# Optimization experiments

Hardware: AMD Instinct MI355X
Metric: run time of the kernel (lower is better)

Reference implementation:

```python
import jax, jax.numpy as jnp
import numpy as np

N = 50000      # nodes
E = 800000     # edges
GENE = 64      # gene_dim
HID = 128      # hidden_dim
NCLS = 10      # num_classes
EPS = 1e-5


def setup_inputs() -> dict:
    key = jax.random.key(0)
    ks = jax.random.split(key, 4)
    inp = {
        "x": jax.random.normal(ks[0], (N, GENE), jnp.float32),
        "edge_index": jax.random.randint(ks[1], (2, E), 0, N),
    }
    # PNA-style conv: concat([x, 4 aggregators x 3 scalers]) -> 13*d_in features
    dims = [(GENE, HID), (HID, 2 * HID), (2 * HID, HID), (HID, HID // 2)]
    for i, (din, dout) in enumerate(dims, 1):
        k = jax.random.fold_in(key, i)
        inp[f"W{i}"] = jax.random.normal(k, (13 * din, dout), jnp.float32) / float(np.sqrt(13 * din))
        inp[f"b{i}"] = jnp.zeros((dout,), jnp.float32)
        inp[f"gamma{i}"] = jnp.ones((dout,), jnp.float32)
        inp[f"beta{i}"] = jnp.zeros((dout,), jnp.float32)
    inp["Wc"] = jax.random.normal(ks[2], (HID // 2, NCLS), jnp.float32) / float(np.sqrt(HID // 2))
    inp["bc"] = jnp.zeros((NCLS,), jnp.float32)
    return inp


def _pna(x, src, dst, deg, log_deg, delta, W, b):
    # gather source features along edges: [E, d]
    msg = x[src]
    cnt = jnp.maximum(deg, 1.0)[:, None]
    s = jax.ops.segment_sum(msg, dst, num_segments=N)
    mean = s / cnt
    mean_sq = jax.ops.segment_sum(msg * msg, dst, num_segments=N) / cnt
    std = jnp.sqrt(jnp.maximum(mean_sq - mean * mean, 0.0) + EPS)
    has = (deg > 0)[:, None]
    mn = jnp.where(has, jax.ops.segment_min(msg, dst, num_segments=N), 0.0)
    mx = jnp.where(has, jax.ops.segment_max(msg, dst, num_segments=N), 0.0)
    aggs = jnp.concatenate([mean, mn, mx, std], axis=-1)  # [N, 4d]
    amp = (log_deg / delta)[:, None]                       # amplification scaler
    att = jnp.where(log_deg > 0, delta / jnp.maximum(log_deg, 1e-6), 1.0)[:, None]
    feat = jnp.concatenate([x, aggs, aggs * amp, aggs * att], axis=-1)  # [N, 13d]
    return feat @ W + b


def _bn(h, gamma, beta):
    m = h.mean(axis=0)
    v = h.var(axis=0)
    return (h - m) / jnp.sqrt(v + EPS) * gamma + beta


def reference(x, edge_index, W1, b1, gamma1, beta1, W2, b2, gamma2, beta2,
              W3, b3, gamma3, beta3, W4, b4, gamma4, beta4, Wc, bc):
    src, dst = edge_index[0], edge_index[1]
    deg = jax.ops.segment_sum(jnp.ones((E,), jnp.float32), dst, num_segments=N)
    log_deg = jnp.log1p(deg)
    delta = log_deg.mean()
    h = _pna(x, src, dst, deg, log_deg, delta, W1, b1)
    h = _bn(jax.nn.relu(h), gamma1, beta1)
    h = _pna(h, src, dst, deg, log_deg, delta, W2, b2)
    h = _bn(jax.nn.relu(h), gamma2, beta2)
    h = _pna(h, src, dst, deg, log_deg, delta, W3, b3)
    h = _bn(jax.nn.relu(h), gamma3, beta3)
    h = _pna(h, src, dst, deg, log_deg, delta, W4, b4)
    h = _bn(jax.nn.relu(h), gamma4, beta4)
    return h @ Wc + bc
```

## Files before the change

kernel.cpp:

```cpp
#include <hip/hip_runtime.h>
#include <hip/hip_bf16.h>

#define NN 50000
#define NE 800000
#define EPSV 1e-5f
#define NB 49

typedef _Float16 h8 __attribute__((ext_vector_type(8)));
typedef float    f4 __attribute__((ext_vector_type(4)));

#define AS1 __attribute__((address_space(1)))
#define AS3 __attribute__((address_space(3)))

__device__ __forceinline__ void gload_lds16(const _Float16* g, _Float16* l){
  __builtin_amdgcn_global_load_lds((const AS1 void*)g, (AS3 void*)l, 16, 0, 0);
}


__global__ void k_deg(const int* __restrict__ dst, int* __restrict__ deg){
  int e = blockIdx.x*blockDim.x + threadIdx.x;
  if(e < NE) atomicAdd(&deg[dst[e]], 1);
}

__global__ void k_logdeg(const int* __restrict__ deg, float* __restrict__ logdeg,
                         float* __restrict__ dsum){
  int i = blockIdx.x*blockDim.x + threadIdx.x;
  float v = 0.f;
  if(i < NN){ v = log1pf((float)deg[i]); logdeg[i] = v; }
  __shared__ float sh[256];
  sh[threadIdx.x] = v; __syncthreads();
  for(int off=128; off>0; off>>=1){
    if(threadIdx.x < off) sh[threadIdx.x] += sh[threadIdx.x+off];
    __syncthreads();
  }
  if(threadIdx.x == 0) atomicAdd(dsum, sh[0]);
}

__global__ void k_scalers(const float* __restrict__ logdeg, const float* __restrict__ dsum,
                          float* __restrict__ amp, float* __restrict__ att){
  int i = blockIdx.x*blockDim.x + threadIdx.x;
  if(i >= NN) return;
  float delta = dsum[0] / (float)NN;
  float ld = logdeg[i];
  amp[i] = ld / delta;
  att[i] = (ld > 0.f) ? (delta / fmaxf(ld, 1e-6f)) : 1.f;
}

__global__ void k_scan1(const int* __restrict__ deg, int* __restrict__ rowptr,
                        int* __restrict__ bsum){
  __shared__ int buf[1024];
  int tid = threadIdx.x;
  int i = blockIdx.x*1024 + tid;
  int v = (i < NN) ? deg[i] : 0;
  buf[tid] = v; __syncthreads();
  for(int off=1; off<1024; off<<=1){
    int t = (tid >= off) ? buf[tid-off] : 0;
    __syncthreads();
    buf[tid] += t;
    __syncthreads();
  }
  if(i < NN) rowptr[i] = buf[tid] - v;
  if(tid == 1023) bsum[blockIdx.x] = buf[1023];
}

__global__ void k_scan2(int* __restrict__ bsum){
  if(threadIdx.x == 0){
    int s = 0;
    for(int b = 0; b < NB; b++){ int t = bsum[b]; bsum[b] = s; s += t; }
    bsum[NB] = s;
  }
}

__global__ void k_scan3(int* __restrict__ rowptr, int* __restrict__ cursor,
                        const int* __restrict__ bsum){
  int i = blockIdx.x*256 + threadIdx.x;
  if(i < NN){
    int v = rowptr[i] + bsum[i >> 10];
    rowptr[i] = v; cursor[i] = v;
  }
  if(i == NN) rowptr[NN] = bsum[NB];
}

__global__ void k_fill(const int* __restrict__ src, const int* __restrict__ dst,
                       int* __restrict__ cursor, int* __restrict__ colidx){
  int e = blockIdx.x*blockDim.x + threadIdx.x;
  if(e < NE){
    int pos = atomicAdd(&cursor[dst[e]], 1);
    colidx[pos] = src[e];
  }
}

__global__ void k_cvtx(const float* __restrict__ x, _Float16* __restrict__ act){
  int i = blockIdx.x*256 + threadIdx.x;
  if(i < NN*64) act[i] = (_Float16)x[i];
}

__global__ void k_coef_id(float* __restrict__ cs, float* __restrict__ csh,
                          _Float16* __restrict__ cs16, _Float16* __restrict__ csh16){
  int c = threadIdx.x;
  cs[c] = 1.f; csh[c] = 0.f;
  cs16[c] = (_Float16)1.f; csh16[c] = (_Float16)0.f;
}

__global__ void k_bn_coef(const float* __restrict__ colsum, const float* __restrict__ colss,
                          const float* __restrict__ gamma, const float* __restrict__ beta,
                          int dout, float* __restrict__ cs, float* __restrict__ csh,
                          _Float16* __restrict__ cs16, _Float16* __restrict__ csh16){
  int c = threadIdx.x;
  if(c >= dout) return;
  float mean = colsum[c] / (float)NN;
  float var  = colss[c] / (float)NN - mean*mean;
  float inv  = rsqrtf(fmaxf(var, 0.f) + EPSV);
  float a = inv * gamma[c];
  float b = beta[c] - mean * a;
  cs[c] = a; csh[c] = b;
  cs16[c] = (_Float16)a; csh16[c] = (_Float16)b;
}


template<int D>
__global__ __launch_bounds__(256) void k_agg8(
    const _Float16* __restrict__ act,
    const int* __restrict__ rowptr, const int* __restrict__ colidx,
    const float* __restrict__ cs, const float* __restrict__ csh,
    _Float16* __restrict__ aggs, size_t aggN)
{
  constexpr int LPN = D >> 3;
  constexpr int NPW = 64 / LPN;
  int wv = threadIdx.x >> 6, lane = threadIdx.x & 63;
  int n = blockIdx.x*(NPW*4) + wv*NPW + (lane / LPN);
  int c = (lane % LPN) * 8;
  if(n >= NN) return;
  int beg = rowptr[n], end = rowptr[n+1];
  const _Float16* hp = act + c;

  float s[8], q[8], mn[8], mx[8];
  #pragma unroll
  for(int j = 0; j < 8; j++){ s[j]=0.f; q[j]=0.f; mn[j]=INFINITY; mx[j]=-INFINITY; }

#define ACC8(v) { _Pragma("unroll") for(int j=0;j<8;j++){ float a=(float)(v)[j]; \
    s[j]+=a; q[j]+=a*a; mn[j]=fminf(mn[j],a); mx[j]=fmaxf(mx[j],a); } }

  int e = beg;
  for(; e+8 <= end; e+=8){
    int i0=colidx[e],   i1=colidx[e+1], i2=colidx[e+2], i3=colidx[e+3];
    int i4=colidx[e+4], i5=colidx[e+5], i6=colidx[e+6], i7=colidx[e+7];
    h8 v0 = *(const h8*)(hp + (size_t)i0*D);
    h8 v1 = *(const h8*)(hp + (size_t)i1*D);
    h8 v2 = *(const h8*)(hp + (size_t)i2*D);
    h8 v3 = *(const h8*)(hp + (size_t)i3*D);
    h8 v4 = *(const h8*)(hp + (size_t)i4*D);
    h8 v5 = *(const h8*)(hp + (size_t)i5*D);
    h8 v6 = *(const h8*)(hp + (size_t)i6*D);
    h8 v7 = *(const h8*)(hp + (size_t)i7*D);
    ACC8(v0) ACC8(v1) ACC8(v2) ACC8(v3) ACC8(v4) ACC8(v5) ACC8(v6) ACC8(v7)
  }
  for(; e+4 <= end; e+=4){
    int i0=colidx[e], i1=colidx[e+1], i2=colidx[e+2], i3=colidx[e+3];
    h8 v0 = *(const h8*)(hp + (size_t)i0*D);
    h8 v1 = *(const h8*)(hp + (size_t)i1*D);
    h8 v2 = *(const h8*)(hp + (size_t)i2*D);
    h8 v3 = *(const h8*)(hp + (size_t)i3*D);
    ACC8(v0) ACC8(v1) ACC8(v2) ACC8(v3)
  }
  for(; e < end; e++){
    h8 v = *(const h8*)(hp + (size_t)colidx[e]*D);
    ACC8(v)
  }
#undef ACC8

  float cnt = (end>beg) ? (float)(end-beg) : 1.f;
  h8 vm, vn, vx, vs;
  #pragma unroll
  for(int j = 0; j < 8; j++){
    float a = cs[c+j], b = csh[c+j];
    float mean_r = s[j]/cnt;
    float var_r  = fmaxf(q[j]/cnt - mean_r*mean_r, 0.f);
    float meanp = a*mean_r + b;
    float mnp = (a >= 0.f) ? a*mn[j]+b : a*mx[j]+b;
    float mxp = (a >= 0.f) ? a*mx[j]+b : a*mn[j]+b;
    float sdp = sqrtf(a*a*var_r + EPSV);
    if(end <= beg){ meanp = 0.f; mnp = 0.f; mxp = 0.f; sdp = sqrtf(EPSV); }
    vm[j] = (_Float16)meanp; vn[j] = (_Float16)mnp;
    vx[j] = (_Float16)mxp;   vs[j] = (_Float16)sdp;
  }

  _Float16* dst = aggs + (size_t)(c>>6)*aggN + (size_t)n*256 + (c & 63);
  *(h8*)(dst)       = vm;
  *(h8*)(dst + 64)  = vn;
  *(h8*)(dst + 128) = vx;
  *(h8*)(dst + 192) = vs;
}


struct PackJob { const float* W; _Float16* dst; int d, o, j0, start; };
struct PackArgs { PackJob job[9]; int total; };

__global__ void k_pack_all(PackArgs a){
  int idx = blockIdx.x*256 + threadIdx.x;
  if(idx >= a.total) return;
  int ji = 0;
  while(ji < 8 && idx >= a.job[ji+1].start) ji++;
  PackJob J = a.job[ji];
  int rel = idx - J.start;
  int j    = rel & 7;
  int lane = (rel >> 3) & 63;
  int rem  = rel >> 9;
  int ntiles = J.o >> 4;
  int kb = rem / ntiles;
  int nt = rem - kb*ntiles;
  int k = kb*32 + (lane>>4)*8 + j;
  int n = nt*16 + (lane&15);
  int srcrow;
  if(k < 64)       srcrow = J.j0 + k;
  else if(k < 320){ int t=k-64;  srcrow = (1+(t>>6))*J.d + J.j0 + (t&63); }
  else if(k < 576){ int t=k-320; srcrow = (5+(t>>6))*J.d + J.j0 + (t&63); }
  else            { int t=k-576; srcrow = (9+(t>>6))*J.d + J.j0 + (t&63); }
  J.dst[rel] = (_Float16)J.W[(size_t)srcrow*J.o + n];
}


template<int NCH>
__global__ __launch_bounds__(256) void k_mfma_fused(
    const _Float16* __restrict__ actIn,
    const _Float16* __restrict__ aggs,
    const float* __restrict__ amp, const float* __restrict__ att,
    const _Float16* __restrict__ cs16, const _Float16* __restrict__ csh16,
    const _Float16* __restrict__ Wp, int o,
    const float* __restrict__ bias,
    _Float16* __restrict__ out,
    float* __restrict__ colsum, float* __restrict__ colss,
    size_t aggN)
{
  constexpr int D = NCH * 64;
  constexpr int NPH = NCH * 9;
  __shared__ _Float16 Bsm[2][12*512];
  __shared__ float redS[64], redQ[64];
  int tid  = threadIdx.x;
  int wv   = tid >> 6;
  int lane = tid & 63;
  int mi   = lane & 15;
  int q    = lane >> 4;

  int T  = gridDim.x * gridDim.y;
  int n_ = blockIdx.y * gridDim.x + blockIdx.x;
  int qq = T >> 3, rr = T & 7, xc = n_ & 7, nl = n_ >> 3;
  int m_ = (xc < rr ? xc*(qq+1) : rr*(qq+1) + (xc-rr)*qq) + nl;
  int bx = m_ % gridDim.x;
  int by = m_ / gridDim.x;

  int m0   = by * 128 + wv * 32;
  int c0   = bx * 64;
  int ntiles = o >> 4;
  int nt0  = bx * 4;

  if(tid < 64){ redS[tid] = 0.f; redQ[tid] = 0.f; }

  int mrow[2];
  mrow[0] = min(m0 + mi,      NN-1);
  mrow[1] = min(m0 + 16 + mi, NN-1);
  _Float16 am16[2] = { (_Float16)amp[mrow[0]], (_Float16)amp[mrow[1]] };
  _Float16 at16[2] = { (_Float16)att[mrow[0]], (_Float16)att[mrow[1]] };
  const _Float16* hAb[2];
  const _Float16* agb[2];
  hAb[0] = actIn + (size_t)mrow[0]*D + q*8;
  hAb[1] = actIn + (size_t)mrow[1]*D + q*8;
  agb[0] = aggs + (size_t)mrow[0]*256 + q*8;
  agb[1] = aggs + (size_t)mrow[1]*256 + q*8;

  f4 acc[2][4] = {};

  auto stageX = [&](_Float16* buf, int c){
    const _Float16* Wpc = Wp + (size_t)c*832*o;
    #pragma unroll
    for(int s = 0; s < 2; s++){
      int ti = wv*2 + s;
      int kb = ti >> 2, nn = ti & 3;
      gload_lds16(Wpc + (((size_t)kb*ntiles + nt0 + nn)*64 + lane)*8,
                  buf + ti*512);
    }
  };
  auto stageP = [&](_Float16* buf, int c, int idx){
    const _Float16* Wpc = Wp + (size_t)c*832*o;
    #pragma unroll
    for(int s = 0; s < 3; s++){
      int ti = wv*3 + s;
      int kj = ti >> 2, nn = ti & 3;
      int kb = (kj == 0 ? 2 : (kj == 1 ? 10 : 18)) + idx;
      gload_lds16(Wpc + (((size_t)kb*ntiles + nt0 + nn)*64 + lane)*8,
                  buf + ti*512);
    }
  };

  h8 pA[2][4]; h8 pS[2][2]; h8 pH[2][2];
  auto loadA = [&](int ph2, int bank){
    if(ph2 >= NPH) return;
    int c = ph2 / 9, sub = ph2 % 9;
    if(sub == 0){
      #pragma unroll
      for(int kb = 0; kb < 2; kb++){
        pS[bank][kb] = *(const h8*)(cs16  + c*64 + kb*32 + q*8);
        pH[bank][kb] = *(const h8*)(csh16 + c*64 + kb*32 + q*8);
        #pragma unroll
        for(int t = 0; t < 2; t++)
          pA[bank][kb*2+t] = *(const h8*)(hAb[t] + c*64 + kb*32);
      }
    } else {
      int idx = sub - 1;
      #pragma unroll
      for(int t = 0; t < 2; t++)
        pA[bank][t] = *(const h8*)(agb[t] + (size_t)c*aggN + idx*32);
    }
  };

  stageX(&Bsm[0][0], 0);
  __builtin_amdgcn_sched_barrier(0);
  loadA(0, 0);
  loadA(1, 1);
  asm volatile("s_waitcnt vmcnt(10)\n\ts_barrier" ::: "memory");

  #pragma unroll
  for(int ph = 0; ph < NPH; ph++){
    const int sub = ph % 9;
    const int bank = ph & 1;
    _Float16* cur = &Bsm[ph & 1][0];
    _Float16* nxt = &Bsm[(ph & 1) ^ 1][0];

    h8 cA[4]; h8 cS[2]; h8 cH[2];
    cA[0] = pA[bank][0]; cA[1] = pA[bank][1];
    if(sub == 0){
      cA[2] = pA[bank][2]; cA[3] = pA[bank][3];
      cS[0] = pS[bank][0]; cS[1] = pS[bank][1];
      cH[0] = pH[bank][0]; cH[1] = pH[bank][1];
    }

    if(ph + 1 < NPH){
      const int c2   = (ph + 1) / 9;
      const int sub2 = (ph + 1) % 9;
      if(sub2 == 0) stageX(nxt, c2);
      else          stageP(nxt, c2, sub2 - 1);
    }
    __builtin_amdgcn_sched_barrier(0);

    loadA(ph + 2, bank);

    __builtin_amdgcn_s_setprio(1);
    if(sub == 0){
      #pragma unroll
      for(int kb = 0; kb < 2; kb++)
        #pragma unroll
        for(int t = 0; t < 2; t++){
          h8 ax = cA[kb*2+t]*cS[kb] + cH[kb];
          #pragma unroll
          for(int nn = 0; nn < 4; nn++)
            acc[t][nn] = __builtin_amdgcn_mfma_f32_16x16x32_f16(
                ax, *(const h8*)(cur + (kb*4+nn)*512 + lane*8), acc[t][nn], 0,0,0);
        }
    } else {
      #pragma unroll
      for(int t = 0; t < 2; t++){
        h8 apl = cA[t];
        h8 aam = apl * am16[t];
        h8 aat = apl * at16[t];
        #pragma unroll
        for(int nn = 0; nn < 4; nn++){
          acc[t][nn] = __builtin_amdgcn_mfma_f32_16x16x32_f16(
              apl, *(const h8*)(cur + (0*4+nn)*512 + lane*8), acc[t][nn], 0,0,0);
          acc[t][nn] = __builtin_amdgcn_mfma_f32_16x16x32_f16(
              aam, *(const h8*)(cur + (4+nn)*512 + lane*8), acc[t][nn], 0,0,0);
          acc[t][nn] = __builtin_amdgcn_mfma_f32_16x16x32_f16(
              aat, *(const h8*)(cur + (8+nn)*512 + lane*8), acc[t][nn], 0,0,0);
        }
      }
    }
    __builtin_amdgcn_s_setprio(0);

    if(ph + 1 < NPH){
      const int ka = (ph + 2 < NPH) ? (((ph + 2) % 9 == 0) ? 8 : 2) : 0;
      if(ka == 8)      asm volatile("s_waitcnt vmcnt(8)\n\ts_barrier" ::: "memory");
      else if(ka == 2) asm volatile("s_waitcnt vmcnt(2)\n\ts_barrier" ::: "memory");
      else             asm volatile("s_waitcnt vmcnt(0)\n\ts_barrier" ::: "memory");
    }
  }

  __syncthreads();

  #pragma unroll
  for(int nn = 0; nn < 4; nn++){
    int n = c0 + nn*16 + mi;
    float bv = bias[n];
    float ps = 0.f, pq = 0.f;
    #pragma unroll
    for(int t = 0; t < 2; t++){
      #pragma unroll
      for(int r = 0; r < 4; r++){
        int m = m0 + t*16 + q*4 + r;
        if(m < NN){
          float v = fmaxf(bv + acc[t][nn][r], 0.f);
          out[(size_t)m*o + n] = (_Float16)v;
          ps += v; pq += v*v;
        }
      }
    }
    ps += __shfl_xor(ps, 16); pq += __shfl_xor(pq, 16);
    ps += __shfl_xor(ps, 32); pq += __shfl_xor(pq, 32);
    if(q == 0){
      atomicAdd(&redS[nn*16 + mi], ps);
      atomicAdd(&redQ[nn*16 + mi], pq);
    }
  }
  __syncthreads();
  if(tid < 64){
    atomicAdd(&colsum[c0 + tid], redS[tid]);
    atomicAdd(&colss[c0 + tid],  redQ[tid]);
  }
}


__global__ __launch_bounds__(256) void k_cls(const _Float16* __restrict__ h,
    const float* __restrict__ cs, const float* __restrict__ csh,
    const float* __restrict__ Wc, const float* __restrict__ bc,
    float* __restrict__ out){
  __shared__ float w[640];
  __shared__ float bb[16];
  __shared__ float sca[64], shb[64];
  int tid = threadIdx.x;
  for(int i = tid; i < 640; i += 256) w[i] = Wc[i];
  if(tid < 10) bb[tid] = bc[tid];
  if(tid < 64){ sca[tid] = cs[tid]; shb[tid] = csh[tid]; }
  __syncthreads();
  int idx = blockIdx.x*256 + tid;
  int n = idx >> 4;
  int c = idx & 15;
  if(n < NN && c < 10){
    float acc = bb[c];
    const _Float16* hp = h + (size_t)n*64;
    #pragma unroll
    for(int k = 0; k < 64; k++)
      acc += ((float)hp[k]*sca[k] + shb[k]) * w[k*10 + c];
    out[(size_t)n*10 + c] = acc;
  }
}


extern "C" void kernel_launch(void* const* d_in, const int* in_sizes, int n_in,
                              void* d_out, int out_size, void* d_ws, size_t ws_size,
                              hipStream_t stream){
  const float* x = (const float*)d_in[0];
  const int* edge = (const int*)d_in[1];
  const int* esrc = edge;
  const int* edst = edge + NE;
  const float* W[4]  = {(const float*)d_in[2],  (const float*)d_in[6],
                        (const float*)d_in[10], (const float*)d_in[14]};
  const float* bb[4] = {(const float*)d_in[3],  (const float*)d_in[7],
                        (const float*)d_in[11], (const float*)d_in[15]};
  const float* gm[4] = {(const float*)d_in[4],  (const float*)d_in[8],
                        (const float*)d_in[12], (const float*)d_in[16]};
  const float* bt[4] = {(const float*)d_in[5],  (const float*)d_in[9],
                        (const float*)d_in[13], (const float*)d_in[17]};
  const float* Wc = (const float*)d_in[18];
  const float* bc = (const float*)d_in[19];
  (void)in_sizes; (void)n_in; (void)out_size; (void)ws_size;

  char* p = (char*)d_ws;
  auto alloc = [&](size_t bytes)->char*{
    char* r = p; p += (bytes + 255) & ~(size_t)255; return r;
  };
  _Float16* act0 = (_Float16*)alloc((size_t)NN*256*2);
  _Float16* act1 = (_Float16*)alloc((size_t)NN*256*2);
  _Float16* aggs = (_Float16*)alloc((size_t)4*NN*256*2);
  int*   deg    = (int*)  alloc((size_t)NN*4);
  float* logdeg = (float*)alloc((size_t)NN*4);
  float* amp    = (float*)alloc((size_t)NN*4);
  float* att    = (float*)alloc((size_t)NN*4);
  int*   rowptr = (int*)  alloc((size_t)(NN+1)*4);
  int*   cursor = (int*)  alloc((size_t)NN*4);
  int*   colidx = (int*)  alloc((size_t)NE*4);
  int*   bsum   = (int*)  alloc((size_t)(NB+1)*4);
  float* colsumL= (float*)alloc(4*256*4);
  float* colssL = (float*)alloc(4*256*4);
  float* dsum   = (float*)alloc(256);
  float*    csA  = (float*)   alloc(256*4);
  float*    cshA = (float*)   alloc(256*4);
  float*    csB  = (float*)   alloc(256*4);
  float*    cshB = (float*)   alloc(256*4);
  _Float16* cs16A  = (_Float16*)alloc(256*2);
  _Float16* csh16A = (_Float16*)alloc(256*2);
  _Float16* cs16B  = (_Float16*)alloc(256*2);
  _Float16* csh16B = (_Float16*)alloc(256*2);

  const int din[4]  = {64, 128, 256, 128};
  const int dto[4]  = {128, 256, 128, 64};
  const size_t aggN = (size_t)NN*256;
  _Float16* WpL[4];
  PackArgs pa; int pj = 0, poff = 0;
  for(int l = 0; l < 4; l++){
    int nch = din[l]/64;
    WpL[l] = (_Float16*)alloc((size_t)nch*832*dto[l]*2);
    for(int c = 0; c < nch; c++){
      pa.job[pj] = { W[l], WpL[l] + (size_t)c*832*dto[l], din[l], dto[l], c*64, poff };
      poff += 832*dto[l]; pj++;
    }
  }
  pa.total = poff;

  hipMemsetAsync(deg, 0, (size_t)NN*4, stream);
  hipMemsetAsync(dsum, 0, 4, stream);
  hipMemsetAsync(colsumL, 0, 4*256*4, stream);
  hipMemsetAsync(colssL,  0, 4*256*4, stream);

  k_pack_all<<<(pa.total+255)/256, 256, 0, stream>>>(pa);
  k_deg     <<<(NE+255)/256, 256, 0, stream>>>(edst, deg);
  k_logdeg  <<<(NN+255)/256, 256, 0, stream>>>(deg, logdeg, dsum);
  k_scalers <<<(NN+255)/256, 256, 0, stream>>>(logdeg, dsum, amp, att);
  k_scan1   <<<NB, 1024, 0, stream>>>(deg, rowptr, bsum);
  k_scan2   <<<1, 64, 0, stream>>>(bsum);
  k_scan3   <<<(NN+256)/256, 256, 0, stream>>>(rowptr, cursor, bsum);
  k_fill    <<<(NE+255)/256, 256, 0, stream>>>(esrc, edst, cursor, colidx);
  k_cvtx    <<<(NN*64+255)/256, 256, 0, stream>>>(x, act0);
  k_coef_id <<<1, 256, 0, stream>>>(csA, cshA, cs16A, csh16A);

  _Float16* actIn = act0;  _Float16* actOut = act1;
  float *csI = csA, *cshI = cshA, *csO = csB, *cshO = cshB;
  _Float16 *cs16I = cs16A, *csh16I = csh16A, *cs16O = cs16B, *csh16O = csh16B;

  for(int l = 0; l < 4; l++){
    int d = din[l], o = dto[l];
    int npb = (64 / (d >> 3)) * 4;
    int nagg = (NN + npb - 1) / npb;
    dim3 g(o/64, (NN+127)/128);
    float* csum = colsumL + l*256;
    float* csq  = colssL + l*256;
    switch(d){
      case 64:
        k_agg8<64><<<nagg, 256, 0, stream>>>(actIn, rowptr, colidx, csI, cshI, aggs, aggN);
        k_mfma_fused<1><<<g, 256, 0, stream>>>(actIn, aggs, amp, att, cs16I, csh16I,
                                               WpL[l], o, bb[l], actOut, csum, csq, aggN);
        break;
      case 128:
        k_agg8<128><<<nagg, 256, 0, stream>>>(actIn, rowptr, colidx, csI, cshI, aggs, aggN);
        k_mfma_fused<2><<<g, 256, 0, stream>>>(actIn, aggs, amp, att, cs16I, csh16I,
                                               WpL[l], o, bb[l], actOut, csum, csq, aggN);
        break;
      default:
        k_agg8<256><<<nagg, 256, 0, stream>>>(actIn, rowptr, colidx, csI, cshI, aggs, aggN);
        k_mfma_fused<4><<<g, 256, 0, stream>>>(actIn, aggs, amp, att, cs16I, csh16I,
                                               WpL[l], o, bb[l], actOut, csum, csq, aggN);
        break;
    }
    k_bn_coef<<<1, 256, 0, stream>>>(csum, csq, gm[l], bt[l], o,
                                     csO, cshO, cs16O, csh16O);
    _Float16* ta = actIn; actIn = actOut; actOut = ta;
    float* tf;
    tf = csI;  csI = csO;  csO = tf;
    tf = cshI; cshI = cshO; cshO = tf;
    _Float16* th;
    th = cs16I;  cs16I = cs16O;  cs16O = th;
    th = csh16I; csh16I = csh16O; csh16O = th;
  }
  k_cls<<<(NN*16+255)/256, 256, 0, stream>>>(actIn, csI, cshI, Wc, bc, (float*)d_out);
}
```

Measured before the change: 650.3 us.

## Templatize MFMA GEMM on M-tile, use 256-row tiles for first three layers

Adds an MT template parameter so each wave handles MT×16 rows, and uses 256-row blocks (MT=4) for layers 0-2 while keeping 128-row blocks for the last layer. The intent is to reuse each staged weight tile across more rows and cut total weight LDS staging traffic. The prefetch pipeline is also simplified from two-deep register prefetch of A to one-phase-ahead loads, with the X-phase loads now issued synchronously, and launch bounds hint 3 blocks/CU for MT=4. Larger tiles raise register pressure and halve the number of blocks, and the shallower prefetch may expose more load latency.

```diff
diff --git a/kernel.cpp b/kernel.cpp
--- a/kernel.cpp
+++ b/kernel.cpp
@@ -220,8 +220,8 @@
 }
 
 
-template<int NCH>
-__global__ __launch_bounds__(256) void k_mfma_fused(
+template<int NCH, int MT>
+__global__ __launch_bounds__(256, (MT==4)?3:1) void k_mfma_fused(
     const _Float16* __restrict__ actIn,
     const _Float16* __restrict__ aggs,
     const float* __restrict__ amp, const float* __restrict__ att,
@@ -249,26 +249,28 @@
   int bx = m_ % gridDim.x;
   int by = m_ / gridDim.x;
 
-  int m0   = by * 128 + wv * 32;
+  int m0   = by * (MT*64) + wv * (MT*16);
   int c0   = bx * 64;
   int ntiles = o >> 4;
   int nt0  = bx * 4;
 
   if(tid < 64){ redS[tid] = 0.f; redQ[tid] = 0.f; }
 
-  int mrow[2];
-  mrow[0] = min(m0 + mi,      NN-1);
-  mrow[1] = min(m0 + 16 + mi, NN-1);
-  _Float16 am16[2] = { (_Float16)amp[mrow[0]], (_Float16)amp[mrow[1]] };
-  _Float16 at16[2] = { (_Float16)att[mrow[0]], (_Float16)att[mrow[1]] };
-  const _Float16* hAb[2];
-  const _Float16* agb[2];
-  hAb[0] = actIn + (size_t)mrow[0]*D + q*8;
-  hAb[1] = actIn + (size_t)mrow[1]*D + q*8;
-  agb[0] = aggs + (size_t)mrow[0]*256 + q*8;
-  agb[1] = aggs + (size_t)mrow[1]*256 + q*8;
-
-  f4 acc[2][4] = {};
+  int mrow[MT];
+  _Float16 am16[MT], at16[MT];
+  const _Float16* hAb[MT];
+  const _Float16* agb[MT];
+  #pragma unroll
+  for(int t = 0; t < MT; t++){
+    mrow[t] = min(m0 + t*16 + mi, NN-1);
+    am16[t] = (_Float16)amp[mrow[t]];
+    at16[t] = (_Float16)att[mrow[t]];
+    hAb[t] = actIn + (size_t)mrow[t]*D + q*8;
+    agb[t] = aggs + (size_t)mrow[t]*256 + q*8;
+  }
+
+  f4 acc[MT][4] = {};
+  h8 pA[MT];
 
   auto stageX = [&](_Float16* buf, int c){
     const _Float16* Wpc = Wp + (size_t)c*832*o;
@@ -276,7 +278,7 @@
     for(int s = 0; s < 2; s++){
       int ti = wv*2 + s;
       int kb = ti >> 2, nn = ti & 3;
-      gload_lds16(Wpc + (((size_t)kb*ntiles + nt0 + nn)*64 + lane)*8,
+      gload_lds16(Wpc + (((size_t)(kb*ntiles + nt0 + nn))*64 + lane)*8,
                   buf + ti*512);
     }
   };
@@ -287,99 +289,89 @@
       int ti = wv*3 + s;
       int kj = ti >> 2, nn = ti & 3;
       int kb = (kj == 0 ? 2 : (kj == 1 ? 10 : 18)) + idx;
-      gload_lds16(Wpc + (((size_t)kb*ntiles + nt0 + nn)*64 + lane)*8,
+      gload_lds16(Wpc + (((size_t)(kb*ntiles + nt0 + nn))*64 + lane)*8,
                   buf + ti*512);
     }
   };
-
-  h8 pA[2][4]; h8 pS[2][2]; h8 pH[2][2];
-  auto loadA = [&](int ph2, int bank){
-    if(ph2 >= NPH) return;
-    int c = ph2 / 9, sub = ph2 % 9;
+  auto loadAgg = [&](int p2){
+    int c2 = p2 / 9, idx = p2 % 9 - 1;
+    #pragma unroll
+    for(int t = 0; t < MT; t++)
+      pA[t] = *(const h8*)(agb[t] + (size_t)c2*aggN + idx*32);
+  };
+
+  stageX(&Bsm[0][0], 0);
+  __builtin_amdgcn_sched_barrier(0);
+  asm volatile("s_waitcnt vmcnt(0)\n\ts_barrier" ::: "memory");
+
+  #pragma unroll
+  for(int ph = 0; ph < NPH; ph++){
+    const int c   = ph / 9;
+    const int sub = ph % 9;
+    _Float16* cur = &Bsm[ph & 1][0];
+    _Float16* nxt = &Bsm[(ph & 1) ^ 1][0];
+    const bool pf = (ph + 1 < NPH) && (((ph + 1) % 9) != 0);
+
     if(sub == 0){
+      if(ph + 1 < NPH) stageP(nxt, c, 0);
+      h8 xs[2], xh[2], xa[2][MT];
       #pragma unroll
       for(int kb = 0; kb < 2; kb++){
-        pS[bank][kb] = *(const h8*)(cs16  + c*64 + kb*32 + q*8);
-        pH[bank][kb] = *(const h8*)(csh16 + c*64 + kb*32 + q*8);
+        xs[kb] = *(const h8*)(cs16  + c*64 + kb*32 + q*8);
+        xh[kb] = *(const h8*)(csh16 + c*64 + kb*32 + q*8);
         #pragma unroll
-        for(int t = 0; t < 2; t++)
-          pA[bank][kb*2+t] = *(const h8*)(hAb[t] + c*64 + kb*32);
-      }
-    } else {
-      int idx = sub - 1;
-      #pragma unroll
-      for(int t = 0; t < 2; t++)
-        pA[bank][t] = *(const h8*)(agb[t] + (size_t)c*aggN + idx*32);
-    }
-  };
-
-  stageX(&Bsm[0][0], 0);
-  __builtin_amdgcn_sched_barrier(0);
-  loadA(0, 0);
-  loadA(1, 1);
-  asm volatile("s_waitcnt vmcnt(10)\n\ts_barrier" ::: "memory");
-
-  #pragma unroll
-  for(int ph = 0; ph < NPH; ph++){
-    const int sub = ph % 9;
-    const int bank = ph & 1;
-    _Float16* cur = &Bsm[ph & 1][0];
-    _Float16* nxt = &Bsm[(ph & 1) ^ 1][0];
-
-    h8 cA[4]; h8 cS[2]; h8 cH[2];
-    cA[0] = pA[bank][0]; cA[1] = pA[bank][1];
-    if(sub == 0){
-      cA[2] = pA[bank][2]; cA[3] = pA[bank][3];
-      cS[0] = pS[bank][0]; cS[1] = pS[bank][1];
-      cH[0] = pH[bank][0]; cH[1] = pH[bank][1];
-    }
-
-    if(ph + 1 < NPH){
-      const int c2   = (ph + 1) / 9;
-      const int sub2 = (ph + 1) % 9;
-      if(sub2 == 0) stageX(nxt, c2);
-      else          stageP(nxt, c2, sub2 - 1);
-    }
-    __builtin_amdgcn_sched_barrier(0);
-
-    loadA(ph + 2, bank);
-
-    __builtin_amdgcn_s_setprio(1);
-    if(sub == 0){
+        for(int t = 0; t < MT; t++)
+          xa[kb][t] = *(const h8*)(hAb[t] + c*64 + kb*32);
+      }
+      __builtin_amdgcn_sched_barrier(0);
+      if(pf) loadAgg(ph + 1);
+      __builtin_amdgcn_s_setprio(1);
       #pragma unroll
       for(int kb = 0; kb < 2; kb++)
         #pragma unroll
-        for(int t = 0; t < 2; t++){
-          h8 ax = cA[kb*2+t]*cS[kb] + cH[kb];
+        for(int t = 0; t < MT; t++){
+          h8 ax = xa[kb][t]*xs[kb] + xh[kb];
           #pragma unroll
           for(int nn = 0; nn < 4; nn++)
             acc[t][nn] = __builtin_amdgcn_mfma_f32_16x16x32_f16(
                 ax, *(const h8*)(cur + (kb*4+nn)*512 + lane*8), acc[t][nn], 0,0,0);
         }
+      __builtin_amdgcn_s_setprio(0);
     } else {
+      h8 cA[MT];
       #pragma unroll
-      for(int t = 0; t < 2; t++){
+      for(int t = 0; t < MT; t++) cA[t] = pA[t];
+      if(ph + 1 < NPH){
+        const int c2 = (ph + 1) / 9, s2 = (ph + 1) % 9;
+        if(s2 == 0) stageX(nxt, c2);
+        else        stageP(nxt, c2, s2 - 1);
+      }
+      __builtin_amdgcn_sched_barrier(0);
+      if(pf) loadAgg(ph + 1);
+      __builtin_amdgcn_s_setprio(1);
+      #pragma unroll
+      for(int t = 0; t < MT; t++){
         h8 apl = cA[t];
         h8 aam = apl * am16[t];
         h8 aat = apl * at16[t];
         #pragma unroll
         for(int nn = 0; nn < 4; nn++){
           acc[t][nn] = __builtin_amdgcn_mfma_f32_16x16x32_f16(
-              apl, *(const h8*)(cur + (0*4+nn)*512 + lane*8), acc[t][nn], 0,0,0);
+              apl, *(const h8*)(cur + nn*512 + lane*8), acc[t][nn], 0,0,0);
           acc[t][nn] = __builtin_amdgcn_mfma_f32_16x16x32_f16(
               aam, *(const h8*)(cur + (4+nn)*512 + lane*8), acc[t][nn], 0,0,0);
           acc[t][nn] = __builtin_amdgcn_mfma_f32_16x16x32_f16(
               aat, *(const h8*)(cur + (8+nn)*512 + lane*8), acc[t][nn], 0,0,0);
         }
       }
-    }
-    __builtin_amdgcn_s_setprio(0);
+      __builtin_amdgcn_s_setprio(0);
+    }
 
     if(ph + 1 < NPH){
-      const int ka = (ph + 2 < NPH) ? (((ph + 2) % 9 == 0) ? 8 : 2) : 0;
-      if(ka == 8)      asm volatile("s_waitcnt vmcnt(8)\n\ts_barrier" ::: "memory");
-      else if(ka == 2) asm volatile("s_waitcnt vmcnt(2)\n\ts_barrier" ::: "memory");
-      else             asm volatile("s_waitcnt vmcnt(0)\n\ts_barrier" ::: "memory");
+      if(pf){
+        if(MT == 4) asm volatile("s_waitcnt vmcnt(4)\n\ts_barrier" ::: "memory");
+        else        asm volatile("s_waitcnt vmcnt(2)\n\ts_barrier" ::: "memory");
+      } else        asm volatile("s_waitcnt vmcnt(0)\n\ts_barrier" ::: "memory");
     }
   }
 
@@ -391,7 +383,7 @@
     float bv = bias[n];
     float ps = 0.f, pq = 0.f;
     #pragma unroll
-    for(int t = 0; t < 2; t++){
+    for(int t = 0; t < MT; t++){
       #pragma unroll
       for(int r = 0; r < 4; r++){
         int m = m0 + t*16 + q*4 + r;
@@ -528,25 +520,37 @@
     int d = din[l], o = dto[l];
     int npb = (64 / (d >> 3)) * 4;
     int nagg = (NN + npb - 1) / npb;
-    dim3 g(o/64, (NN+127)/128);
     float* csum = colsumL + l*256;
     float* csq  = colssL + l*256;
-    switch(d){
-      case 64:
+    switch(l){
+      case 0: {
+        dim3 g(o/64, (NN+255)/256);
         k_agg8<64><<<nagg, 256, 0, stream>>>(actIn, rowptr, colidx, csI, cshI, aggs, aggN);
-        k_mfma_fused<1><<<g, 256, 0, stream>>>(actIn, aggs, amp, att, cs16I, csh16I,
-                                               WpL[l], o, bb[l], actOut, csum, csq, aggN);
+        k_mfma_fused<1,4><<<g, 256, 0, stream>>>(actIn, aggs, amp, att, cs16I, csh16I,
+                                                 WpL[l], o, bb[l], actOut, csum, csq, aggN);
         break;
-      case 128:
+      }
+      case 1: {
+        dim3 g(o/64, (NN+255)/256);
         k_agg8<128><<<nagg, 256, 0, stream>>>(actIn, rowptr, colidx, csI, cshI, aggs, aggN);
-        k_mfma_fused<2><<<g, 256, 0, stream>>>(actIn, aggs, amp, att, cs16I, csh16I,
-                                               WpL[l], o, bb[l], actOut, csum, csq, aggN);
+        k_mfma_fused<2,4><<<g, 256, 0, stream>>>(actIn, aggs, amp, att, cs16I, csh16I,
+                                                 WpL[l], o, bb[l], actOut, csum, csq, aggN);
         break;
-      default:
+      }
+      case 2: {
+        dim3 g(o/64, (NN+255)/256);
         k_agg8<256><<<nagg, 256, 0, stream>>>(actIn, rowptr, colidx, csI, cshI, aggs, aggN);
-        k_mfma_fused<4><<<g, 256, 0, stream>>>(actIn, aggs, amp, att, cs16I, csh16I,
-                                               WpL[l], o, bb[l], actOut, csum, csq, aggN);
+        k_mfma_fused<4,4><<<g, 256, 0, stream>>>(actIn, aggs, amp, att, cs16I, csh16I,
+                                                 WpL[l], o, bb[l], actOut, csum, csq, aggN);
         break;
+      }
+      default: {
+        dim3 g(o/64, (NN+127)/128);
+        k_agg8<128><<<nagg, 256, 0, stream>>>(actIn, rowptr, colidx, csI, cshI, aggs, aggN);
+        k_mfma_fused<2,2><<<g, 256, 0, stream>>>(actIn, aggs, amp, att, cs16I, csh16I,
+                                                 WpL[l], o, bb[l], actOut, csum, csq, aggN);
+        break;
+      }
     }
     k_bn_coef<<<1, 256, 0, stream>>>(csum, csq, gm[l], bt[l], o,
                                      csO, cshO, cs16O, csh16O);
```

Measured after the change: 894.5 us. +37.6%, slower.
